# Performance work log

Measured on AMD Instinct MI355X. Metric: run time of the kernel, lower is better.

## Reference

```python
import jax, jax.numpy as jnp
import numpy as np

B, L, H, HEADS = 4, 2048, 512, 8
D = H // HEADS  # 64


def setup_inputs() -> dict:
    key = jax.random.key(0)
    ks = jax.random.split(key, 13)
    s = 0.02
    return {
        "q_in": jax.random.normal(ks[0], (B, L, H), jnp.float32),
        "k_in": jax.random.normal(ks[1], (B, L, H), jnp.float32),
        "v_in": jax.random.normal(ks[2], (B, L, H), jnp.float32),
        "Wq_w": jax.random.normal(ks[3], (H, H), jnp.float32) * s,
        "Wq_b": jax.random.normal(ks[4], (H,), jnp.float32) * s,
        "Wk_w": jax.random.normal(ks[5], (H, H), jnp.float32) * s,
        "Wk_b": jax.random.normal(ks[6], (H,), jnp.float32) * s,
        "Wv_w": jax.random.normal(ks[7], (H, H), jnp.float32) * s,
        "Wv_b": jax.random.normal(ks[8], (H,), jnp.float32) * s,
        "Wo_w": jax.random.normal(ks[9], (H, H), jnp.float32) * s,
        "Wo_b": jax.random.normal(ks[10], (H,), jnp.float32) * s,
        "Wp_w": jax.random.normal(ks[11], (2 * L - 1, D), jnp.float32) * s,
        "Wp_b": jax.random.normal(ks[12], (2 * L - 1,), jnp.float32) * s,
    }


def _skew(p):
    # p: (b, h, l, 2l-1) -> relative-position bias (b, h, l, l) via pad/flatten/reshape skew trick
    b, h, l, _ = p.shape
    p = jnp.pad(p, ((0, 0), (0, 0), (0, 0), (0, 1)))          # (b,h,l,2l)
    p = p.reshape(b, h, 2 * l * l)
    p = jnp.pad(p, ((0, 0), (0, 0), (0, l - 1)))               # (b,h,(l+1)(2l-1))
    p = p.reshape(b, h, l + 1, 2 * l - 1)
    return p[:, :, :-1, -l:]                                   # (b,h,l,l)


def reference(q_in, k_in, v_in, Wq_w, Wq_b, Wk_w, Wk_b, Wv_w, Wv_b, Wo_w, Wo_b, Wp_w, Wp_b):
    b, l, hid = q_in.shape
    q = q_in @ Wq_w.T + Wq_b
    k = k_in @ Wk_w.T + Wk_b
    v = v_in @ Wv_w.T + Wv_b
    # (b, l, h*d) -> (b, h, l, d)
    to_heads = lambda x: x.reshape(b, l, HEADS, D).transpose(0, 2, 1, 3)
    q, k, v = to_heads(q), to_heads(k), to_heads(v)
    q = q / jnp.sqrt(jnp.asarray(D, q.dtype))  # scaling applied BEFORE posenc, as in original
    scores = jnp.einsum('bhid,bhjd->bhij', q, k)
    pos = _skew(q @ Wp_w.T + Wp_b)             # posenc linear applied to scaled q
    scores = scores + pos
    attn = jax.nn.softmax(scores, axis=-1)     # (b,h,l,l)
    # Original torch.einsum('b h l l, b h l d -> b h l d') takes the DIAGONAL of attn
    diag = jnp.diagonal(attn, axis1=-2, axis2=-1)  # (b,h,l)
    out = diag[..., None] * v                       # (b,h,l,d)
    out = out.transpose(0, 2, 1, 3).reshape(b, l, hid)
    return out @ Wo_w.T + Wo_b
```

## Files before the change

kernel.cpp:

```cpp
#include <hip/hip_runtime.h>
#include <cstdint>


typedef unsigned short u16;
typedef __bf16 bf16x8 __attribute__((ext_vector_type(8)));
typedef __bf16 bf16x2 __attribute__((ext_vector_type(2)));
typedef float  f32x16 __attribute__((ext_vector_type(16)));
typedef uint32_t __attribute__((address_space(1))) as1_u32;
typedef uint32_t __attribute__((address_space(3))) as3_u32;

__device__ __forceinline__ u16 f2bf(float f) {
  __bf16 h = (__bf16)f;
  return __builtin_bit_cast(u16, h);
}
__device__ __forceinline__ uint32_t pkbf(float a, float b) {
  bf16x2 v; v[0] = (__bf16)a; v[1] = (__bf16)b;
  return __builtin_bit_cast(uint32_t, v);
}
__device__ __forceinline__ float bf2f(u16 u) {
  return __uint_as_float(((uint32_t)u) << 16);
}
__device__ __forceinline__ float exp2v(float x) {
  float r;
  asm("v_exp_f32 %0, %1" : "=v"(r) : "v"(x));
  return r;
}
__device__ __forceinline__ void gl_lds16(const void* g, void* l) {
  __builtin_amdgcn_global_load_lds((const as1_u32*)g, (as3_u32*)l, 16, 0, 0);
}

__global__ __launch_bounds__(256) void prep_kernel(
    const float* __restrict__ qin, const float* __restrict__ kin, const float* __restrict__ vin,
    const float* __restrict__ wq,  const float* __restrict__ wk,  const float* __restrict__ wv,
    const float* __restrict__ wo,  const float* __restrict__ wp,
    u16* __restrict__ xq, u16* __restrict__ xk, u16* __restrict__ xv,
    u16* __restrict__ bwq, u16* __restrict__ bwk, u16* __restrict__ bwv,
    u16* __restrict__ bwo, u16* __restrict__ bwp) {
  long u = (long)blockIdx.x * 256 + threadIdx.x;
  const float* src; u16* dst; long off; float qs = 1.0f;
  if      (u < 524288L)  { src = qin; dst = xq;  off = u; }
  else if (u < 1048576L) { src = kin; dst = xk;  off = u - 524288L; }
  else if (u < 1572864L) { src = vin; dst = xv;  off = u - 1048576L; }
  else if (u < 1605632L) { src = wq;  dst = bwq; off = u - 1572864L; qs = 0.18033688f; }
  else if (u < 1638400L) { src = wk;  dst = bwk; off = u - 1605632L; }
  else if (u < 1671168L) { src = wv;  dst = bwv; off = u - 1638400L; }
  else if (u < 1703936L) { src = wo;  dst = bwo; off = u - 1671168L; }
  else if (u < 1736696L) { src = wp;  dst = bwp; off = u - 1703936L; }
  else {
    long o = (u - 1736696L) * 8 + 262080L;
    uint4 z = {0u, 0u, 0u, 0u};
    *(uint4*)(bwp + o) = z;
    return;
  }
  const float4* s4 = (const float4*)(src + off * 8);
  float4 a = s4[0], b = s4[1];
  uint32_t p0 = pkbf(a.x * qs, a.y * qs);
  uint32_t p1 = pkbf(a.z * qs, a.w * qs);
  uint32_t p2 = pkbf(b.x * qs, b.y * qs);
  uint32_t p3 = pkbf(b.z * qs, b.w * qs);
  uint4 o = {p0, p1, p2, p3};
  *(uint4*)(dst + off * 8) = o;
}

__device__ __forceinline__ void gemm64_core(
    const u16* __restrict__ A, const u16* __restrict__ W, int m0, int n0,
    u16* Al, u16* Bl, int tid, f32x16& acc) {
  const int lane = tid & 63, w = tid >> 6;
  const int wi = w >> 1, wj = w & 1;
  const int l31 = lane & 31, lh = lane >> 5;
  const int r = tid >> 2, ch = tid & 3;
  const int gch = ch ^ ((r >> 1) & 3);
  for (int kb = 0; kb < 16; ++kb) {
    gl_lds16(A + (long)(m0 + r) * 512 + kb * 32 + gch * 8, (char*)Al + w * 64 * 16);
    gl_lds16(W + (long)(n0 + r) * 512 + kb * 32 + gch * 8, (char*)Bl + w * 64 * 16);
    __syncthreads();
    bf16x8 af[2], bfr[2];
#pragma unroll
    for (int ks = 0; ks < 2; ++ks) {
      int c2 = 2 * ks + lh;
      int rA = 32 * wi + l31;
      int rB = 32 * wj + l31;
      af[ks]  = *(const bf16x8*)((char*)Al + (rA * 4 + (c2 ^ ((rA >> 1) & 3))) * 16);
      bfr[ks] = *(const bf16x8*)((char*)Bl + (rB * 4 + (c2 ^ ((rB >> 1) & 3))) * 16);
    }
#pragma unroll
    for (int ks = 0; ks < 2; ++ks)
      acc = __builtin_amdgcn_mfma_f32_32x32x16_bf16(af[ks], bfr[ks], acc, 0, 0, 0);
    __syncthreads();
  }
}

__global__ __launch_bounds__(256, 4) void gemm_bt(
    const u16* __restrict__ A, const u16* __restrict__ W, const float* __restrict__ bias,
    float* __restrict__ ofp) {
  __shared__ u16 Al[64 * 32];
  __shared__ u16 Bl[64 * 32];
  const int tid = threadIdx.x;
  const int lane = tid & 63, w = tid >> 6;
  const int wi = w >> 1, wj = w & 1;
  const int l31 = lane & 31, lh = lane >> 5;
  const int u = (blockIdx.x & 7) * 128 + (blockIdx.x >> 3);
  const int m0 = (u >> 3) * 64, n0 = (u & 7) * 64;

  float bv = bias[n0 + 32 * wj + l31];
  f32x16 acc;
#pragma unroll
  for (int rr = 0; rr < 16; ++rr) acc[rr] = bv;

  gemm64_core(A, W, m0, n0, Al, Bl, tid, acc);

  int n = n0 + 32 * wj + l31;
#pragma unroll
  for (int rr = 0; rr < 16; ++rr) {
    int row = m0 + 32 * wi + (rr & 3) + 8 * (rr >> 2) + 4 * lh;
    ofp[(long)row * 512 + n] = acc[rr];
  }
}

__global__ __launch_bounds__(256, 4) void qkv_gemm(
    const u16* __restrict__ xq, const u16* __restrict__ xk, const u16* __restrict__ xv,
    const u16* __restrict__ wqp, const u16* __restrict__ wkp, const u16* __restrict__ wvp,
    const float* __restrict__ bq, const float* __restrict__ bk, const float* __restrict__ bv,
    u16* __restrict__ oq, u16* __restrict__ ok, u16* __restrict__ ov) {
  __shared__ u16 Al[64 * 32];
  __shared__ u16 Bl[64 * 32];
  const int mat = blockIdx.x >> 10;
  const int t = blockIdx.x & 1023;
  const u16* A = (mat == 0) ? xq : (mat == 1) ? xk : xv;
  const u16* W = (mat == 0) ? wqp : (mat == 1) ? wkp : wvp;
  const float* bias = (mat == 0) ? bq : (mat == 1) ? bk : bv;
  u16* obf = (mat == 0) ? oq : (mat == 1) ? ok : ov;
  const float bsc = (mat == 0) ? 0.18033688f : 1.0f;

  const int tid = threadIdx.x;
  const int lane = tid & 63, w = tid >> 6;
  const int wi = w >> 1, wj = w & 1;
  const int l31 = lane & 31, lh = lane >> 5;
  const int u = (t & 7) * 128 + (t >> 3);
  const int m0 = (u >> 3) * 64, n0 = (u & 7) * 64;

  float bvv = bias[n0 + 32 * wj + l31] * bsc;
  f32x16 acc;
#pragma unroll
  for (int rr = 0; rr < 16; ++rr) acc[rr] = bvv;

  gemm64_core(A, W, m0, n0, Al, Bl, tid, acc);

  int n = n0 + 32 * wj + l31;
  int h = n >> 6, d = n & 63;
#pragma unroll
  for (int rr = 0; rr < 16; ++rr) {
    int row = m0 + 32 * wi + (rr & 3) + 8 * (rr >> 2) + 4 * lh;
    int b = row >> 11, l = row & 2047;
    obf[(((long)(b * 8 + h)) * 2048 + l) * 64 + d] = f2bf(acc[rr]);
  }
}

__global__ __launch_bounds__(256, 3) void attn_kernel(
    const u16* __restrict__ qw, const u16* __restrict__ kw, const u16* __restrict__ vw,
    const u16* __restrict__ wpw, const float* __restrict__ wpb, u16* __restrict__ outp) {
  __shared__ u16 Pl[283 * 66];
  __shared__ float sdiag[64];
  __shared__ float rssum[128];
  __shared__ float attw[64];

  const int tid = threadIdx.x, lane = tid & 63, w = tid >> 6;
  const int wi = w >> 1, wj = w & 1;
  const int sbi = blockIdx.x;
  const int kk_ = sbi >> 3;
  const int bh = (sbi & 7) + 8 * (kk_ >> 5);
  const int it = kk_ & 31;
  const int i0 = it * 64, base = 1984 - i0;
  const u16* qb = qw + (long)bh * 2048 * 64;
  const u16* kb = kw + (long)bh * 2048 * 64;
  const u16* vb = vw + (long)bh * 2048 * 64;

  const int l31 = lane & 31, lh = lane >> 5;
  const int iibase = 32 * wi + 4 * lh;

  bf16x8 aq[4];
  {
    int row = i0 + 32 * wi + l31;
    const u16* p = qb + (long)row * 64 + lh * 8;
#pragma unroll
    for (int kk = 0; kk < 4; ++kk) aq[kk] = *(const bf16x8*)(p + kk * 16);
  }

  float rsum[16];
#pragma unroll
  for (int r = 0; r < 16; ++r) rsum[r] = 0.f;

  const int browc = base + 32 * wj + l31;

  auto ldbias = [&](int g) -> float {
    int brow = browc + 64 * g;
    int bidx = brow > 4094 ? 4094 : brow;
    return wpb[bidx] * 1.44269504f;
  };

  auto pblock = [&](int g, float bv) {
    const u16* bp = wpw + (long)(browc + 64 * g) * 64 + lh * 8;
    bf16x8 bw[4];
#pragma unroll
    for (int kk = 0; kk < 4; ++kk) bw[kk] = *(const bf16x8*)(bp + kk * 16);
    f32x16 accP;
#pragma unroll
    for (int r = 0; r < 16; ++r) accP[r] = bv;
#pragma unroll
    for (int kk = 0; kk < 4; ++kk)
      accP = __builtin_amdgcn_mfma_f32_32x32x16_bf16(aq[kk], bw[kk], accP, 0, 0, 0);
    int colp = (g & 3) * 64 + 32 * wj + l31;
    uint32_t pk0[8];
#pragma unroll
    for (int m = 0; m < 4; ++m) {
      pk0[2 * m]     = pkbf(accP[4 * m + 0], accP[4 * m + 1]);
      pk0[2 * m + 1] = pkbf(accP[4 * m + 2], accP[4 * m + 3]);
    }
    u16* wl = &Pl[colp * 66 + iibase];
#pragma unroll
    for (int m = 0; m < 4; ++m) {
      *(uint32_t*)(wl + 8 * m) = pk0[2 * m];
      *(uint32_t*)(wl + 8 * m + 2) = pk0[2 * m + 1];
    }
    if (((g & 3) == 0) && (wj == 0) && (l31 < 27)) {
      u16* wl2 = wl + 256 * 66;
#pragma unroll
      for (int m = 0; m < 4; ++m) {
        *(uint32_t*)(wl2 + 8 * m) = pk0[2 * m];
        *(uint32_t*)(wl2 + 8 * m + 2) = pk0[2 * m + 1];
      }
    }
  };

  pblock(0, ldbias(0));
  pblock(1, ldbias(1));
  float bvc = ldbias(2);
  __syncthreads();

  const int W1c = 63 + 32 * wj + l31 - iibase;
  uint32_t pc[16];
  {
    int b_ = ((W1c - 27) & 255) + 27;
    const u16* rb = &Pl[b_ * 66 + iibase - 27 * 65];
#pragma unroll
    for (int r = 0; r < 16; ++r) {
      const int lrr = (r & 3) + 8 * (r >> 2);
      pc[r] = rb[(27 - lrr) * 65];
    }
  }

  for (int jt = 0; jt < 32; ++jt) {
    bf16x8 kf[4];
    {
      const u16* bp = kb + (long)(jt * 64 + 32 * wj + l31) * 64 + lh * 8;
#pragma unroll
      for (int kk = 0; kk < 4; ++kk) kf[kk] = *(const bf16x8*)(bp + kk * 16);
    }
    float bvn = (jt <= 29) ? ldbias(jt + 3) : 0.f;
    if (jt <= 30) pblock(jt + 2, bvc);
    __syncthreads();

    uint32_t pn[16];
    if (jt <= 30) {
      int W1 = 64 * (jt + 1) + W1c;
      int b_ = ((W1 - 27) & 255) + 27;
      const u16* rb = &Pl[b_ * 66 + iibase - 27 * 65];
#pragma unroll
      for (int r = 0; r < 16; ++r) {
        const int lrr = (r & 3) + 8 * (r >> 2);
        pn[r] = rb[(27 - lrr) * 65];
      }
    }

    f32x16 accS;
#pragma unroll
    for (int r = 0; r < 16; ++r) accS[r] = __uint_as_float(pc[r] << 16);
#pragma unroll
    for (int kk = 0; kk < 4; ++kk)
      accS = __builtin_amdgcn_mfma_f32_32x32x16_bf16(aq[kk], kf[kk], accS, 0, 0, 0);
#pragma unroll
    for (int r = 0; r < 16; ++r) rsum[r] += exp2v(accS[r]);

    if ((jt == it) && (wi == wj)) {
#pragma unroll
      for (int r = 0; r < 16; ++r) {
        const int lrr = (r & 3) + 8 * (r >> 2);
        if ((lrr + 4 * lh) == l31) sdiag[32 * wi + l31] = accS[r];
      }
    }
#pragma unroll
    for (int r = 0; r < 16; ++r) pc[r] = pn[r];
    bvc = bvn;
  }

#pragma unroll
  for (int r = 0; r < 16; ++r) {
    float v = rsum[r];
    v += __shfl_xor(v, 1);
    v += __shfl_xor(v, 2);
    v += __shfl_xor(v, 4);
    v += __shfl_xor(v, 8);
    v += __shfl_xor(v, 16);
    rsum[r] = v;
  }
  if (l31 == 0) {
#pragma unroll
    for (int r = 0; r < 16; ++r) {
      int lr = (r & 3) + 8 * (r >> 2) + 4 * lh;
      rssum[(32 * wi + lr) * 2 + wj] = rsum[r];
    }
  }
  __syncthreads();
  if (tid < 64) {
    float S = rssum[2 * tid] + rssum[2 * tid + 1];
    attw[tid] = exp2v(sdiag[tid]) / S;
  }
  __syncthreads();
  {
    int r = tid >> 2, dd = (tid & 3) * 16;
    float a = attw[r];
    int b = bh >> 3, h = bh & 7;
    const u16* vp = vb + (long)(i0 + r) * 64 + dd;
    u16* op = outp + ((long)(b * 2048 + i0 + r)) * 512 + h * 64 + dd;
    uint4 v0 = *(const uint4*)vp;
    uint4 v1 = *(const uint4*)(vp + 8);
    uint32_t vin[8] = {v0.x, v0.y, v0.z, v0.w, v1.x, v1.y, v1.z, v1.w};
    uint32_t vout[8];
#pragma unroll
    for (int e = 0; e < 8; ++e) {
      float lo = bf2f((u16)(vin[e] & 0xffffu)) * a;
      float hi = bf2f((u16)(vin[e] >> 16)) * a;
      vout[e] = pkbf(lo, hi);
    }
    uint4 o0 = {vout[0], vout[1], vout[2], vout[3]};
    uint4 o1 = {vout[4], vout[5], vout[6], vout[7]};
    *(uint4*)op = o0;
    *(uint4*)(op + 8) = o1;
  }
}

extern "C" void kernel_launch(void* const* d_in, const int* in_sizes, int n_in,
                              void* d_out, int out_size, void* d_ws, size_t ws_size,
                              hipStream_t stream) {
  (void)in_sizes; (void)n_in; (void)out_size; (void)ws_size;
  const float* q_in = (const float*)d_in[0];
  const float* k_in = (const float*)d_in[1];
  const float* v_in = (const float*)d_in[2];
  const float* Wq_w = (const float*)d_in[3];
  const float* Wq_b = (const float*)d_in[4];
  const float* Wk_w = (const float*)d_in[5];
  const float* Wk_b = (const float*)d_in[6];
  const float* Wv_w = (const float*)d_in[7];
  const float* Wv_b = (const float*)d_in[8];
  const float* Wo_w = (const float*)d_in[9];
  const float* Wo_b = (const float*)d_in[10];
  const float* Wp_w = (const float*)d_in[11];
  const float* Wp_b = (const float*)d_in[12];

  char* ws = (char*)d_ws;
  u16* xq   = (u16*)(ws + 0);
  u16* xk   = (u16*)(ws + 8388608);
  u16* xv   = (u16*)(ws + 16777216);
  u16* wq   = (u16*)(ws + 25165824);
  u16* wk   = (u16*)(ws + 25690112);
  u16* wv   = (u16*)(ws + 26214400);
  u16* wo   = (u16*)(ws + 26738688);
  u16* wp   = (u16*)(ws + 27262976);
  u16* q_ws = (u16*)(ws + 27787264);
  u16* k_ws = (u16*)(ws + 36175872);
  u16* v_ws = (u16*)(ws + 44564480);
  u16* opre = (u16*)(ws + 52953088);

  prep_kernel<<<6784, 256, 0, stream>>>(q_in, k_in, v_in, Wq_w, Wk_w, Wv_w, Wo_w, Wp_w,
                                        xq, xk, xv, wq, wk, wv, wo, wp);
  qkv_gemm<<<3072, 256, 0, stream>>>(xq, xk, xv, wq, wk, wv, Wq_b, Wk_b, Wv_b,
                                     q_ws, k_ws, v_ws);
  attn_kernel<<<1024, 256, 0, stream>>>(q_ws, k_ws, v_ws, wp, Wp_b, opre);
  gemm_bt<<<1024, 256, 0, stream>>>(opre, wo, Wo_b, (float*)d_out);
}
```

Baseline: 273.5 us.

## Replace LDS skew buffer with register-resident position tiles and ds_bpermute

```diff
diff --git a/kernel.cpp b/kernel.cpp
--- a/kernel.cpp
+++ b/kernel.cpp
@@ -159,7 +159,6 @@
 __global__ __launch_bounds__(256, 3) void attn_kernel(
     const u16* __restrict__ qw, const u16* __restrict__ kw, const u16* __restrict__ vw,
     const u16* __restrict__ wpw, const float* __restrict__ wpb, u16* __restrict__ outp) {
-  __shared__ u16 Pl[283 * 66];
   __shared__ float sdiag[64];
   __shared__ float rssum[128];
   __shared__ float attw[64];
@@ -170,18 +169,22 @@
   const int kk_ = sbi >> 3;
   const int bh = (sbi & 7) + 8 * (kk_ >> 5);
   const int it = kk_ & 31;
-  const int i0 = it * 64, base = 1984 - i0;
+  const int i0 = it * 64;
   const u16* qb = qw + (long)bh * 2048 * 64;
   const u16* kb = kw + (long)bh * 2048 * 64;
   const u16* vb = vw + (long)bh * 2048 * 64;
 
   const int l31 = lane & 31, lh = lane >> 5;
-  const int iibase = 32 * wi + 4 * lh;
+  const int r0 = i0 + 32 * wi;
+  const int c0b = 1024 * wj;
+  const int wb = 2016 + c0b - r0;
+  const int tsel = l31 + 4 * lh;
+  const int lbb = l31 + 31 - 4 * lh;
+  const int hb = 128 * lh;
 
   bf16x8 aq[4];
   {
-    int row = i0 + 32 * wi + l31;
-    const u16* p = qb + (long)row * 64 + lh * 8;
+    const u16* p = qb + (long)(r0 + l31) * 64 + lh * 8;
 #pragma unroll
     for (int kk = 0; kk < 4; ++kk) aq[kk] = *(const bf16x8*)(p + kk * 16);
   }
@@ -190,108 +193,72 @@
 #pragma unroll
   for (int r = 0; r < 16; ++r) rsum[r] = 0.f;
 
-  const int browc = base + 32 * wj + l31;
-
-  auto ldbias = [&](int g) -> float {
-    int brow = browc + 64 * g;
-    int bidx = brow > 4094 ? 4094 : brow;
-    return wpb[bidx] * 1.44269504f;
+  int td = -1;
+  {
+    int tdn = r0 - c0b;
+    if (tdn >= 0 && tdn < 1024) td = tdn >> 5;
+  }
+
+  auto ptile = [&](int widx, f32x16& P) {
+    int wr = widx + l31;
+    const u16* bp = wpw + (long)wr * 64 + lh * 8;
+    bf16x8 bw[4];
+#pragma unroll
+    for (int kk = 0; kk < 4; ++kk) bw[kk] = *(const bf16x8*)(bp + kk * 16);
+    float bv = wpb[wr > 4094 ? 4094 : wr] * 1.44269504f;
+#pragma unroll
+    for (int r = 0; r < 16; ++r) P[r] = bv;
+#pragma unroll
+    for (int kk = 0; kk < 4; ++kk)
+      P = __builtin_amdgcn_mfma_f32_32x32x16_bf16(aq[kk], bw[kk], P, 0, 0, 0);
   };
 
-  auto pblock = [&](int g, float bv) {
-    const u16* bp = wpw + (long)(browc + 64 * g) * 64 + lh * 8;
-    bf16x8 bw[4];
-#pragma unroll
-    for (int kk = 0; kk < 4; ++kk) bw[kk] = *(const bf16x8*)(bp + kk * 16);
-    f32x16 accP;
-#pragma unroll
-    for (int r = 0; r < 16; ++r) accP[r] = bv;
-#pragma unroll
-    for (int kk = 0; kk < 4; ++kk)
-      accP = __builtin_amdgcn_mfma_f32_32x32x16_bf16(aq[kk], bw[kk], accP, 0, 0, 0);
-    int colp = (g & 3) * 64 + 32 * wj + l31;
-    uint32_t pk0[8];
-#pragma unroll
-    for (int m = 0; m < 4; ++m) {
-      pk0[2 * m]     = pkbf(accP[4 * m + 0], accP[4 * m + 1]);
-      pk0[2 * m + 1] = pkbf(accP[4 * m + 2], accP[4 * m + 3]);
-    }
-    u16* wl = &Pl[colp * 66 + iibase];
-#pragma unroll
-    for (int m = 0; m < 4; ++m) {
-      *(uint32_t*)(wl + 8 * m) = pk0[2 * m];
-      *(uint32_t*)(wl + 8 * m + 2) = pk0[2 * m + 1];
-    }
-    if (((g & 3) == 0) && (wj == 0) && (l31 < 27)) {
-      u16* wl2 = wl + 256 * 66;
-#pragma unroll
-      for (int m = 0; m < 4; ++m) {
-        *(uint32_t*)(wl2 + 8 * m) = pk0[2 * m];
-        *(uint32_t*)(wl2 + 8 * m + 2) = pk0[2 * m + 1];
-      }
-    }
-  };
-
-  pblock(0, ldbias(0));
-  pblock(1, ldbias(1));
-  float bvc = ldbias(2);
-  __syncthreads();
-
-  const int W1c = 63 + 32 * wj + l31 - iibase;
-  uint32_t pc[16];
-  {
-    int b_ = ((W1c - 27) & 255) + 27;
-    const u16* rb = &Pl[b_ * 66 + iibase - 27 * 65];
+  f32x16 P0, P1, P2;
+  ptile(wb, P0);
+  ptile(wb + 32, P1);
+
+  auto step = [&](int t, f32x16& PA, f32x16& PB, f32x16& PN, bool last) {
+    int c0 = c0b + 32 * t;
+    const u16* kp = kb + (long)(c0 + l31) * 64 + lh * 8;
+    bf16x8 kf[4];
+#pragma unroll
+    for (int kk = 0; kk < 4; ++kk) kf[kk] = *(const bf16x8*)(kp + kk * 16);
+
+    f32x16 accS;
 #pragma unroll
     for (int r = 0; r < 16; ++r) {
       const int lrr = (r & 3) + 8 * (r >> 2);
-      pc[r] = rb[(27 - lrr) * 65];
-    }
-  }
-
-  for (int jt = 0; jt < 32; ++jt) {
-    bf16x8 kf[4];
-    {
-      const u16* bp = kb + (long)(jt * 64 + 32 * wj + l31) * 64 + lh * 8;
-#pragma unroll
-      for (int kk = 0; kk < 4; ++kk) kf[kk] = *(const bf16x8*)(bp + kk * 16);
-    }
-    float bvn = (jt <= 29) ? ldbias(jt + 3) : 0.f;
-    if (jt <= 30) pblock(jt + 2, bvc);
-    __syncthreads();
-
-    uint32_t pn[16];
-    if (jt <= 30) {
-      int W1 = 64 * (jt + 1) + W1c;
-      int b_ = ((W1 - 27) & 255) + 27;
-      const u16* rb = &Pl[b_ * 66 + iibase - 27 * 65];
+      float M = (tsel >= 31 - lrr) ? PA[r] : PB[r];
+      int gi = __builtin_amdgcn_ds_bpermute((((lbb - lrr) & 31) << 2) + hb,
+                                            __float_as_int(M));
+      accS[r] = __int_as_float(gi);
+    }
+
+    if (!last) ptile(wb + 32 * (t + 2), PN);
+
+#pragma unroll
+    for (int kk = 0; kk < 4; ++kk)
+      accS = __builtin_amdgcn_mfma_f32_32x32x16_bf16(aq[kk], kf[kk], accS, 0, 0, 0);
+
+#pragma unroll
+    for (int r = 0; r < 16; ++r) rsum[r] += exp2v(accS[r]);
+
+    if (t == td) {
 #pragma unroll
       for (int r = 0; r < 16; ++r) {
         const int lrr = (r & 3) + 8 * (r >> 2);
-        pn[r] = rb[(27 - lrr) * 65];
+        if (l31 == lrr + 4 * lh) sdiag[32 * wi + l31] = accS[r];
       }
     }
-
-    f32x16 accS;
-#pragma unroll
-    for (int r = 0; r < 16; ++r) accS[r] = __uint_as_float(pc[r] << 16);
-#pragma unroll
-    for (int kk = 0; kk < 4; ++kk)
-      accS = __builtin_amdgcn_mfma_f32_32x32x16_bf16(aq[kk], kf[kk], accS, 0, 0, 0);
-#pragma unroll
-    for (int r = 0; r < 16; ++r) rsum[r] += exp2v(accS[r]);
-
-    if ((jt == it) && (wi == wj)) {
-#pragma unroll
-      for (int r = 0; r < 16; ++r) {
-        const int lrr = (r & 3) + 8 * (r >> 2);
-        if ((lrr + 4 * lh) == l31) sdiag[32 * wi + l31] = accS[r];
-      }
-    }
-#pragma unroll
-    for (int r = 0; r < 16; ++r) pc[r] = pn[r];
-    bvc = bvn;
-  }
+  };
+
+  for (int tt = 0; tt < 30; tt += 3) {
+    step(tt,     P0, P1, P2, false);
+    step(tt + 1, P1, P2, P0, false);
+    step(tt + 2, P2, P0, P1, false);
+  }
+  step(30, P0, P1, P2, false);
+  step(31, P1, P2, P0, true);
 
 #pragma unroll
   for (int r = 0; r < 16; ++r) {
```

New measurement: 302.6 us. 1.11x slower.
